# Performance work log

Measured on AMD Instinct MI355X. Metric: run time of the kernel, lower is better.

The kernel has to match this reference:

```python
import jax, jax.numpy as jnp
import numpy as np

N_EMBD = 1024
N_HEAD = 16
HEAD_DIM = N_EMBD // N_HEAD
BLOCK_SIZE = 2048
ROPE_BASE = 10000.0


def _rope_tables(dim, max_len, base=ROPE_BASE):
    half = dim // 2
    freqs = 1.0 / base ** (jnp.arange(half, dtype=jnp.float32) / half)
    angles = jnp.arange(max_len, dtype=jnp.float32)[:, None] * freqs[None, :]  # (T, half)
    return jnp.cos(angles), jnp.sin(angles)


def _apply_rope(x, cos, sin):
    # x: (B, H, T, D); cos/sin: (T, D//2)
    T = x.shape[2]
    c = cos[:T][None, None]
    s = sin[:T][None, None]
    x1 = x[..., ::2]
    x2 = x[..., 1::2]
    out = jnp.stack([x1 * c - x2 * s, x1 * s + x2 * c], axis=-1)  # (B,H,T,D//2,2)
    return out.reshape(x.shape)


def setup_inputs() -> dict:
    key = jax.random.key(0)
    k1, k2, k3, k4, k5 = jax.random.split(key, 5)
    B, T, C = 2, 2048, N_EMBD
    x = jax.random.normal(k1, (B, T, C), dtype=jnp.float32)
    scale = 1.0 / np.sqrt(C)
    Wqkv = jax.random.normal(k2, (C, 3 * C), dtype=jnp.float32) * scale
    bqkv = jax.random.normal(k3, (3 * C,), dtype=jnp.float32) * 0.01
    Wproj = jax.random.normal(k4, (C, C), dtype=jnp.float32) * scale
    bproj = jax.random.normal(k5, (C,), dtype=jnp.float32) * 0.01
    cos, sin = _rope_tables(HEAD_DIM, BLOCK_SIZE)
    return {"x": x, "Wqkv": Wqkv, "bqkv": bqkv, "Wproj": Wproj, "bproj": bproj,
            "cos": cos, "sin": sin}


def reference(x, Wqkv, bqkv, Wproj, bproj, cos, sin):
    B, T, C = x.shape
    H, D = N_HEAD, HEAD_DIM
    qkv = x @ Wqkv + bqkv  # (B,T,3C)
    q, k, v = jnp.split(qkv, 3, axis=-1)
    # (B,T,C) -> (B,H,T,D)
    q = q.reshape(B, T, H, D).transpose(0, 2, 1, 3)
    k = k.reshape(B, T, H, D).transpose(0, 2, 1, 3)
    v = v.reshape(B, T, H, D).transpose(0, 2, 1, 3)
    q = _apply_rope(q, cos, sin)
    k = _apply_rope(k, cos, sin)
    att = jnp.einsum('bhtd,bhsd->bhts', q, k) * (D ** -0.5)
    causal = jnp.tril(jnp.ones((T, T), dtype=bool))
    att = jnp.where(causal[None, None], att, -jnp.inf)
    att = jax.nn.softmax(att, axis=-1)
    y = jnp.einsum('bhts,bhsd->bhtd', att, v)  # (B,H,T,D)
    y = y.transpose(0, 2, 1, 3).reshape(B, T, C)
    return y @ Wproj + bproj
```

## Files before the change

### kernel.cpp

```cpp
#include <hip/hip_runtime.h>
#include <stdint.h>

typedef short s16x8 __attribute__((ext_vector_type(8)));
typedef float f32x4 __attribute__((ext_vector_type(4)));
typedef unsigned short u16;
typedef unsigned int u32;

__device__ __forceinline__ float bf2f(u16 u) {
  union { u32 i; float f; } v; v.i = ((u32)u) << 16; return v.f;
}
__device__ __forceinline__ u16 f2bf(float f) {
  union { float f; u32 i; } v; v.f = f;
  u32 i = v.i;
  return (u16)((i + 0x7fffu + ((i >> 16) & 1u)) >> 16);
}
__device__ __forceinline__ u16 f2bf_fast(float f) {
  union { float f; u32 i; } v; v.f = f;
  return (u16)((v.i + 0x8000u) >> 16);
}

__device__ __forceinline__ s16x8 load8(const void* p, size_t idx, int isf32) {
  s16x8 r;
  if (isf32) {
    const float* f = (const float*)p + idx;
    f32x4 a = *(const f32x4*)f;
    f32x4 b = *(const f32x4*)(f + 4);
#pragma unroll
    for (int j = 0; j < 4; j++) {
      r[j] = (short)f2bf(a[j]);
      r[4 + j] = (short)f2bf(b[j]);
    }
  } else {
    r = *(const s16x8*)((const u16*)p + idx);
  }
  return r;
}
__device__ __forceinline__ float loadf(const void* p, size_t idx, int isf32) {
  return isf32 ? ((const float*)p)[idx] : bf2f(((const u16*)p)[idx]);
}

__device__ __forceinline__ void cp16(const u16* g, u16* l) {
  __builtin_amdgcn_global_load_lds(
      (const __attribute__((address_space(1))) u32*)g,
      (__attribute__((address_space(3))) u32*)l, 16, 0, 0);
}

__global__ void detect_dtype(const u16* __restrict__ x, int* __restrict__ flags) {
  int cnt = 0;
  for (int i = threadIdx.x; i < 4096; i += 64) {
    int e = (x[i] >> 7) & 0xFF;
    if (e >= 0xF0) cnt++;
  }
  unsigned long long any = __ballot(cnt > 0);
  if (threadIdx.x == 0) {
    flags[0] = (any != 0ull) ? 1 : 0;
    flags[1] = 0;
  }
}

__global__ __launch_bounds__(256) void convert_x(const void* __restrict__ x,
                                                 const int* __restrict__ fp,
                                                 u16* __restrict__ xb) {
  int tid = blockIdx.x * 256 + threadIdx.x;
  int r = tid & 127, kq = (tid >> 7) & 3, kB = (tid >> 9) & 31, mB = tid >> 14;
  size_t src = (size_t)(mB * 128 + r) * 1024 + kB * 32 + kq * 8;
  *(s16x8*)(xb + (size_t)tid * 8) = load8(x, src, *fp);
}

__global__ __launch_bounds__(256) void transposeW2(
    const void* __restrict__ Wqkv, const void* __restrict__ Wproj,
    const int* __restrict__ fp, u16* __restrict__ WqkvT,
    u16* __restrict__ WprojT) {
  __shared__ u32 tile32[32 * 66];
  const int f = *fp;
  const int tid = threadIdx.x;
  const int bx = blockIdx.x;
  const void* W;
  u16* WT;
  int N, nb, qkvSide;
  if (bx < 48) { W = Wqkv; WT = WqkvT; N = 3072; nb = bx * 64; qkvSide = 1; }
  else         { W = Wproj; WT = WprojT; N = 1024; nb = (bx - 48) * 64; qkvSide = 0; }
  const int kb = blockIdx.y * 64;
  {
    int a = tid >> 3, c8 = tid & 7;
    s16x8 r0 = load8(W, (size_t)(kb + 2 * a) * N + nb + c8 * 8, f);
    s16x8 r1 = load8(W, (size_t)(kb + 2 * a + 1) * N + nb + c8 * 8, f);
#pragma unroll
    for (int j = 0; j < 8; j++)
      tile32[a * 66 + c8 * 8 + j] = (u32)(u16)r0[j] | ((u32)(u16)r1[j] << 16);
  }
  __syncthreads();
#pragma unroll
  for (int i = 0; i < 2; i++) {
    int idx = tid + i * 256;
    int n = idx & 63, c8 = idx >> 6;
    s16x8 v;
#pragma unroll
    for (int w = 0; w < 4; w++) {
      u32 pk = tile32[(c8 * 4 + w) * 66 + n];
      v[2 * w] = (short)(u16)(pk & 0xFFFF);
      v[2 * w + 1] = (short)(u16)(pk >> 16);
    }
    int R = nb + n, k = kb + c8 * 8;
    int kB = k >> 5, kq = (k >> 3) & 3;
    size_t off;
    if (qkvSide) {
      int nB = R >> 7, r = R & 127;
      off = ((size_t)(nB * 32 + kB) * 4 + kq) * 1024 + r * 8;
    } else {
      int nB = R >> 6, r = R & 63;
      off = (size_t)(nB * 32 + kB) * 2048 + kq * 512 + r * 8;
    }
    *(s16x8*)(WT + off) = v;
  }
}

__global__ __launch_bounds__(256) void transposeV(const u16* __restrict__ qkv,
                                                  u16* __restrict__ vT) {
  __shared__ u32 tile32[64 * 33];
  const int tid = threadIdx.x;
  const int tb = blockIdx.x * 64, bh = blockIdx.y;
  const int b = bh >> 4, h = bh & 15;
  {
    int a = tid >> 3, c8 = tid & 7;
    const u16* base = qkv + (size_t)(b * 2048 + tb + 2 * a) * 3072 + 2048 + h * 64;
    s16x8 r0 = *(const s16x8*)(base + c8 * 8);
    s16x8 r1 = *(const s16x8*)(base + 3072 + c8 * 8);
#pragma unroll
    for (int j = 0; j < 8; j++)
      tile32[(c8 * 8 + j) * 33 + a] = (u32)(u16)r0[j] | ((u32)(u16)r1[j] << 16);
  }
  __syncthreads();
#pragma unroll
  for (int i = 0; i < 2; i++) {
    int idx = tid + i * 256;
    int d = idx >> 3, c8 = idx & 7;
    s16x8 v;
#pragma unroll
    for (int w = 0; w < 4; w++) {
      u32 pk = tile32[d * 33 + c8 * 4 + w];
      v[2 * w] = (short)(u16)(pk & 0xFFFF);
      v[2 * w + 1] = (short)(u16)(pk >> 16);
    }
    *(s16x8*)(vT + ((size_t)bh * 64 + d) * 2048 + tb + c8 * 8) = v;
  }
}

template <int MB, int NT, int KK, int ATILED, int BK>
__global__ __launch_bounds__(256, 6) void gemm_bt(
    const u16* __restrict__ A, int lda, const u16* __restrict__ Bt,
    const void* __restrict__ bias, const int* __restrict__ fI32,
    void* __restrict__ C, int ropeMode, int outF,
    const void* __restrict__ cost, const void* __restrict__ sint, int N) {
  constexpr int MT = MB / 32;
  constexpr int NTW = NT / 32;
  constexpr int KSUB = BK / 32;
  constexpr int KT = KK / BK;
  constexpr int APW = MB / 64;
  constexpr int BPW = NT / 64;
  __shared__ __attribute__((aligned(16))) u16 As[KSUB * MB * 32];
  __shared__ __attribute__((aligned(16))) u16 Bs[KSUB * NT * 32];
  const int inf32 = *fI32;
  const int tid = threadIdx.x;
  const int wave = tid >> 6, lane = tid & 63, quad = lane >> 4, l16 = lane & 15;
  const int bx = blockIdx.x, by = blockIdx.y;
  const int m0 = by * MB, n0 = bx * NT;
  const int wm = (wave & 1) * (MB / 2), wn = (wave >> 1) * (NT / 2);
  f32x4 acc[MT][NTW];
#pragma unroll
  for (int i = 0; i < MT; i++)
#pragma unroll
    for (int j = 0; j < NTW; j++) acc[i][j] = (f32x4){0.f, 0.f, 0.f, 0.f};

  const u16* aT = nullptr;
  const u16* aP = nullptr;
  int halfA = 0;
  if constexpr (ATILED) {
    const int mB = (MB == 128) ? by : (by >> 1);
    halfA = (MB == 128) ? 0 : (by & 1);
    aT = A + (size_t)mB * KK * 128 + lane * 8;
  } else {
    const int lr = lane >> 2, lk = (lane & 3) * 8;
    aP = A + (size_t)(m0 + wave * (MB / 4) + lr) * lda + lk;
  }
  const u16* bT = Bt + (size_t)bx * KK * NT + lane * 8;

  for (int s = 0; s < KT; ++s) {
    __syncthreads();
#pragma unroll
    for (int ks = 0; ks < KSUB; ks++) {
      const int kb32 = s * KSUB + ks;
      if constexpr (ATILED) {
#pragma unroll
        for (int j = 0; j < APW; j++) {
          const int c = wave * APW + j;
          size_t off;
          if constexpr (MB == 128) off = (size_t)kb32 * 4096 + c * 512;
          else                     off = (size_t)kb32 * 4096 + c * 1024 + halfA * 512;
          cp16(aT + off, As + ks * (MB * 32) + c * 512);
        }
      } else {
#pragma unroll
        for (int j = 0; j < APW; j++)
          cp16(aP + kb32 * 32 + (size_t)(16 * j) * lda,
               As + ks * (MB * 32) + wave * (APW * 512) + j * 512);
      }
#pragma unroll
      for (int j = 0; j < BPW; j++) {
        const int c = wave * BPW + j;
        cp16(bT + (size_t)kb32 * (NT * 32) + c * 512,
             Bs + ks * (NT * 32) + c * 512);
      }
    }
    __syncthreads();
#pragma unroll
    for (int ks = 0; ks < KSUB; ks++) {
      s16x8 af[MT], bfr[NTW];
#pragma unroll
      for (int mt = 0; mt < MT; mt++) {
        if constexpr (ATILED)
          af[mt] = *(const s16x8*)(As + ks * (MB * 32) + quad * (MB * 8) +
                                   (wm + mt * 16 + l16) * 8);
        else
          af[mt] = *(const s16x8*)(As + ks * (MB * 32) +
                                   (wm + mt * 16 + l16) * 32 + quad * 8);
      }
#pragma unroll
      for (int nt = 0; nt < NTW; nt++)
        bfr[nt] = *(const s16x8*)(Bs + ks * (NT * 32) + quad * (NT * 8) +
                                  (wn + nt * 16 + l16) * 8);
#pragma unroll
      for (int mt = 0; mt < MT; mt++)
#pragma unroll
        for (int nt = 0; nt < NTW; nt++)
          acc[mt][nt] = __builtin_amdgcn_mfma_f32_16x16x32_bf16(
              af[mt], bfr[nt], acc[mt][nt], 0, 0, 0);
    }
  }

#pragma unroll
  for (int nt = 0; nt < NTW; nt++) {
    int col = n0 + wn + nt * 16 + l16;
    float bv = loadf(bias, col, inf32);
    if (ropeMode && col < 2048) {
      int j = (col & 63) >> 1, odd = col & 1;
#pragma unroll
      for (int mt = 0; mt < MT; mt++)
#pragma unroll
        for (int r = 0; r < 4; r++) {
          int row = m0 + wm + mt * 16 + quad * 4 + r, t = row & 2047;
          float cv = loadf(cost, (size_t)t * 32 + j, inf32);
          float sv = loadf(sint, (size_t)t * 32 + j, inf32);
          float val = acc[mt][nt][r] + bv;
          float pr = __shfl_xor(val, 1);
          float res = odd ? (pr * sv + val * cv) : (val * cv - pr * sv);
          ((u16*)C)[(size_t)row * N + col] = f2bf(res);
        }
    } else if (outF && inf32) {
#pragma unroll
      for (int mt = 0; mt < MT; mt++)
#pragma unroll
        for (int r = 0; r < 4; r++) {
          int row = m0 + wm + mt * 16 + quad * 4 + r;
          ((float*)C)[(size_t)row * N + col] = acc[mt][nt][r] + bv;
        }
    } else {
#pragma unroll
      for (int mt = 0; mt < MT; mt++)
#pragma unroll
        for (int r = 0; r < 4; r++) {
          int row = m0 + wm + mt * 16 + quad * 4 + r;
          ((u16*)C)[(size_t)row * N + col] = f2bf(acc[mt][nt][r] + bv);
        }
    }
  }
}

__device__ __forceinline__ int kvIdx(int chunk, int row) {
  return chunk * 512 + (((row & 56) | ((row ^ chunk) & 7)) << 3);
}
__device__ __forceinline__ int pIdx(int chunk, int row) {
  return chunk * 128 + (((row & 8) | ((row ^ chunk) & 7)) << 3);
}

__global__ __launch_bounds__(512) void attn_kernel(u16* qkv,
                                                   const u16* __restrict__ vT) {
  __shared__ __attribute__((aligned(16))) u16 Ks[8 * 512];
  __shared__ __attribute__((aligned(16))) u16 Vt[8 * 512];
  __shared__ __attribute__((aligned(16))) u16 Pl[8][8 * 128];
  const int tid = threadIdx.x;
  const int wave = tid >> 6, lane = tid & 63, quad = lane >> 4, l16 = lane & 15;
  const int cu = blockIdx.x & 255, round = blockIdx.x >> 8;
  const int p = cu >> 5, bh = cu & 31;
  const int qt = round ? p : 15 - p;
  const int h = bh & 15;
  const size_t rb = (size_t)(bh >> 4) * 2048;
  const int qb = qt * 128;
  const float SCALE = 0.18033688011112042f;

  s16x8 qa0, qa1;
  {
    const u16* qp = qkv + (rb + qb + wave * 16 + l16) * 3072 + h * 64;
    qa0 = *(const s16x8*)(qp + quad * 8);
    qa1 = *(const s16x8*)(qp + 32 + quad * 8);
  }

  f32x4 o[4];
  float l_r[4] = {0.f, 0.f, 0.f, 0.f};
#pragma unroll
  for (int i = 0; i < 4; i++) o[i] = (f32x4){0.f, 0.f, 0.f, 0.f};

  const int nchunks = 2 * qt + 2;
  const int srow = tid >> 3, sc8 = tid & 7;
  const int stIdx = kvIdx(sc8, srow);
  s16x8 kr, vr;
  {
    kr = *(const s16x8*)(qkv + (rb + srow) * 3072 + 1024 + h * 64 + sc8 * 8);
    vr = *(const s16x8*)(vT + ((size_t)bh * 64 + srow) * 2048 + sc8 * 8);
  }

  for (int c = 0; c < nchunks; c++) {
    const int sb = c * 64;
    __syncthreads();
    *(s16x8*)(Ks + stIdx) = kr;
    *(s16x8*)(Vt + stIdx) = vr;
    __syncthreads();
    if (c + 1 < nchunks) {
      const int nb = sb + 64;
      kr = *(const s16x8*)(qkv + (rb + nb + srow) * 3072 + 1024 + h * 64 +
                           sc8 * 8);
      vr = *(const s16x8*)(vT + ((size_t)bh * 64 + srow) * 2048 + nb + sc8 * 8);
    }

    if (sb > qb + wave * 16 + 15) continue;

    f32x4 S[4];
#pragma unroll
    for (int kf = 0; kf < 4; kf++) {
      s16x8 k0 = *(const s16x8*)(Ks + kvIdx(quad, kf * 16 + l16));
      s16x8 k1 = *(const s16x8*)(Ks + kvIdx(quad + 4, kf * 16 + l16));
      f32x4 a = (f32x4){0.f, 0.f, 0.f, 0.f};
      a = __builtin_amdgcn_mfma_f32_16x16x32_bf16(qa0, k0, a, 0, 0, 0);
      a = __builtin_amdgcn_mfma_f32_16x16x32_bf16(qa1, k1, a, 0, 0, 0);
      S[kf] = a;
    }

    u16* P = Pl[wave];
    const int mq = qb + wave * 16;
    const bool needMask = (sb + 63) > mq;
#pragma unroll
    for (int r = 0; r < 4; r++) {
      const int qi = mq + quad * 4 + r;
#pragma unroll
      for (int kf = 0; kf < 4; kf++) {
        float pv = __builtin_amdgcn_exp2f(S[kf][r] * SCALE);
        if (needMask) pv = ((sb + kf * 16 + l16) <= qi) ? pv : 0.f;
        l_r[r] += pv;
        P[pIdx(kf * 2 + (l16 >> 3), quad * 4 + r) + (l16 & 7)] = f2bf_fast(pv);
      }
    }
    asm volatile("s_waitcnt lgkmcnt(0)" ::: "memory");
    s16x8 pa0 = *(const s16x8*)(P + pIdx(quad, l16));
    s16x8 pa1 = *(const s16x8*)(P + pIdx(quad + 4, l16));

#pragma unroll
    for (int dt = 0; dt < 4; dt++) {
      s16x8 vb0 = *(const s16x8*)(Vt + kvIdx(quad, dt * 16 + l16));
      s16x8 vb1 = *(const s16x8*)(Vt + kvIdx(quad + 4, dt * 16 + l16));
      o[dt] = __builtin_amdgcn_mfma_f32_16x16x32_bf16(pa0, vb0, o[dt], 0, 0, 0);
      o[dt] = __builtin_amdgcn_mfma_f32_16x16x32_bf16(pa1, vb1, o[dt], 0, 0, 0);
    }
  }

  float inv[4];
#pragma unroll
  for (int r = 0; r < 4; r++) {
    float rs = l_r[r];
#pragma unroll
    for (int off = 8; off; off >>= 1) rs += __shfl_xor(rs, off);
    inv[r] = 1.0f / fmaxf(rs, 1e-30f);
  }
#pragma unroll
  for (int dt = 0; dt < 4; dt++)
#pragma unroll
    for (int r = 0; r < 4; r++)
      qkv[(rb + qb + wave * 16 + quad * 4 + r) * 3072 + 2048 + h * 64 +
          dt * 16 + l16] = f2bf(o[dt][r] * inv[r]);
}

extern "C" void kernel_launch(void* const* d_in, const int* in_sizes, int n_in,
                              void* d_out, int out_size, void* d_ws,
                              size_t ws_size, hipStream_t stream) {
  const void* x = d_in[0];
  const void* Wqkv = d_in[1];
  const void* bqkv = d_in[2];
  const void* Wproj = d_in[3];
  const void* bproj = d_in[4];
  const void* cost = d_in[5];
  const void* sint = d_in[6];

  int* flags = (int*)d_ws;
  u16* WqkvT = (u16*)d_ws + 128;
  u16* WprojT = WqkvT + (size_t)3072 * 1024;
  u16* qkv = WprojT + (size_t)1024 * 1024;
  u16* yb = qkv + 2048;
  u16* xb = (u16*)d_out;
  u16* vT = (u16*)d_out + (size_t)4096 * 1024;

  detect_dtype<<<1, 64, 0, stream>>>((const u16*)x, flags);
  convert_x<<<2048, 256, 0, stream>>>(x, flags, xb);
  transposeW2<<<dim3(64, 16), 256, 0, stream>>>(Wqkv, Wproj, flags, WqkvT,
                                                WprojT);
  gemm_bt<64, 128, 1024, 1, 64><<<dim3(24, 64), 256, 0, stream>>>(
      xb, 1024, WqkvT, bqkv, flags, qkv, 1, 0, cost, sint, 3072);
  transposeV<<<dim3(32, 32), 256, 0, stream>>>(qkv, vT);
  attn_kernel<<<512, 512, 0, stream>>>(qkv, vT);
  gemm_bt<64, 64, 1024, 0, 64><<<dim3(16, 64), 256, 0, stream>>>(
      yb, 3072, WprojT, bproj, flags, d_out, 0, 1, nullptr, nullptr, 1024);
}
```

Baseline: 212.5 us.

## Write attention output in MFMA-tiled layout for projection GEMM A loads

The attention kernel now scatters its output into a tiled layout that matches the shared-memory fragment order the GEMM expects. A new ATILED==2 mode in the projection GEMM copies one contiguous 16-byte chunk per lane straight into LDS. This removes the strided row-major A loads and lets A fragments be read in the tiled LDS pattern, which should cut bank conflicts. In exchange, the attention epilogue's global stores are more scattered, and the layout is tied to the fixed 3072 stride and 128-row grouping.

```diff
diff --git a/kernel.cpp b/kernel.cpp
--- a/kernel.cpp
+++ b/kernel.cpp
@@ -174,11 +174,15 @@
 
   const u16* aT = nullptr;
   const u16* aP = nullptr;
-  int halfA = 0;
-  if constexpr (ATILED) {
-    const int mB = (MB == 128) ? by : (by >> 1);
+  int mBv = 0, halfA = 0;
+  if constexpr (ATILED == 1) {
+    mBv = (MB == 128) ? by : (by >> 1);
     halfA = (MB == 128) ? 0 : (by & 1);
-    aT = A + (size_t)mB * KK * 128 + lane * 8;
+    aT = A + (size_t)mBv * KK * 128 + lane * 8;
+  } else if constexpr (ATILED == 2) {
+    mBv = by >> 1;
+    halfA = by & 1;
+    aT = A + lane * 8;
   } else {
     const int lr = lane >> 2, lk = (lane & 3) * 8;
     aP = A + (size_t)(m0 + wave * (MB / 4) + lr) * lda + lk;
@@ -190,7 +194,7 @@
 #pragma unroll
     for (int ks = 0; ks < KSUB; ks++) {
       const int kb32 = s * KSUB + ks;
-      if constexpr (ATILED) {
+      if constexpr (ATILED == 1) {
 #pragma unroll
         for (int j = 0; j < APW; j++) {
           const int c = wave * APW + j;
@@ -199,6 +203,10 @@
           else                     off = (size_t)kb32 * 4096 + c * 1024 + halfA * 512;
           cp16(aT + off, As + ks * (MB * 32) + c * 512);
         }
+      } else if constexpr (ATILED == 2) {
+        const int vr = mBv * 128 + kb32 * 4 + wave;
+        cp16(aT + (size_t)vr * 3072 + halfA * 512,
+             As + ks * (MB * 32) + wave * 512);
       } else {
 #pragma unroll
         for (int j = 0; j < APW; j++)
@@ -218,7 +226,7 @@
       s16x8 af[MT], bfr[NTW];
 #pragma unroll
       for (int mt = 0; mt < MT; mt++) {
-        if constexpr (ATILED)
+        if constexpr (ATILED != 0)
           af[mt] = *(const s16x8*)(As + ks * (MB * 32) + quad * (MB * 8) +
                                    (wm + mt * 16 + l16) * 8);
         else
@@ -383,9 +391,13 @@
 #pragma unroll
   for (int dt = 0; dt < 4; dt++)
 #pragma unroll
-    for (int r = 0; r < 4; r++)
-      qkv[(rb + qb + wave * 16 + quad * 4 + r) * 3072 + 2048 + h * 64 +
-          dt * 16 + l16] = f2bf(o[dt][r] * inv[r]);
+    for (int r = 0; r < 4; r++) {
+      const int grow = (int)rb + qb + wave * 16 + quad * 4 + r;
+      const int col = h * 64 + dt * 16 + l16;
+      const int vrow = (grow >> 7) * 128 + (col >> 5) * 4 + ((col >> 3) & 3);
+      qkv[(size_t)vrow * 3072 + 2048 + (grow & 127) * 8 + (col & 7)] =
+          f2bf(o[dt][r] * inv[r]);
+    }
 }
 
 extern "C" void kernel_launch(void* const* d_in, const int* in_sizes, int n_in,
@@ -415,6 +427,6 @@
       xb, 1024, WqkvT, bqkv, flags, qkv, 1, 0, cost, sint, 3072);
   transposeV<<<dim3(32, 32), 256, 0, stream>>>(qkv, vT);
   attn_kernel<<<512, 512, 0, stream>>>(qkv, vT);
-  gemm_bt<64, 64, 1024, 0, 64><<<dim3(16, 64), 256, 0, stream>>>(
+  gemm_bt<64, 64, 1024, 2, 64><<<dim3(16, 64), 256, 0, stream>>>(
       yb, 3072, WprojT, bproj, flags, d_out, 0, 1, nullptr, nullptr, 1024);
 }
```

New measurement: 198.1 us. 6.8% less time.
